# Kernel optimization log

Hardware: AMD Instinct MI355X
Metric: run time of the kernel (lower is better)

Reference implementation:

```python
import jax, jax.numpy as jnp
import numpy as np

HEADS = 8
NUM_CLASS = 4
DIM = 512


def setup_inputs() -> dict:
    key = jax.random.key(0)
    k0, k1, k2, k3 = jax.random.split(key, 4)
    B, N, C = 4, 1280, DIM  # N = (NUM_CLASS+1) * 256 tokens per group
    x = jax.random.normal(k0, (B, N, C), jnp.float32)
    # modality-presence mask: 1 = modality available, 0 = missing
    mask = jax.random.randint(k1, (B, NUM_CLASS), 0, 2).astype(jnp.int32)
    s = 1.0 / np.sqrt(C)
    W_qkv = jax.random.normal(k2, (C, 3 * C), jnp.float32) * s  # qkv (no bias)
    W_proj = jax.random.normal(k3, (C, C), jnp.float32) * s
    b_proj = jnp.zeros((C,), jnp.float32)
    return {"x": x, "mask": mask, "W_qkv": W_qkv, "W_proj": W_proj, "b_proj": b_proj}


def reference(x, mask, W_qkv, W_proj, b_proj):
    B, N, C = x.shape
    H = HEADS
    hd = C // H
    scale = hd ** -0.5
    # qkv: [B,N,3C] -> [3,B,H,N,hd]
    qkv = (x @ W_qkv).reshape(B, N, 3, H, hd).transpose(2, 0, 3, 1, 4)
    q, k, v = qkv[0], qkv[1], qkv[2]
    attn = jnp.einsum('bhqd,bhkd->bhqk', q, k) * scale  # [B,H,N,N]
    # block mask: keys belonging to missing modality groups are disallowed;
    # the last (fusion) group is always allowed -> every row has valid keys.
    np_ = N // (NUM_CLASS + 1)  # tokens per group
    group = jnp.arange(N) // np_  # [N], group id in [0, NUM_CLASS]
    allowed = jnp.concatenate(
        [mask.astype(jnp.float32), jnp.ones((B, 1), jnp.float32)], axis=1)  # [B, NUM_CLASS+1]
    col_ok = allowed[:, group]  # [B, N] per-key allowance
    attn = jnp.where(col_ok[:, None, None, :] == 0, -jnp.inf, attn)
    attn = jax.nn.softmax(attn, axis=-1)
    out = jnp.einsum('bhqk,bhkd->bhqd', attn, v)  # [B,H,N,hd]
    out = out.transpose(0, 2, 1, 3).reshape(B, N, C)
    out = out @ W_proj + b_proj
    return out, attn
```

## Files before the change

### kernel.cpp

```cpp
#include <hip/hip_runtime.h>
#include <math.h>

#define BATCH 4
#define NSEQ  1280
#define CDIM  512
#define HEADS 8
#define HD    64
#define NT    20
#define NQT   20

typedef __attribute__((ext_vector_type(8))) short bf16x8;
typedef __attribute__((ext_vector_type(4))) float f32x4;
typedef __attribute__((ext_vector_type(4))) unsigned short us4;

#define MFMA16(a,b,c) __builtin_amdgcn_mfma_f32_16x16x32_bf16(a,b,c,0,0,0)

__device__ __forceinline__ unsigned short f2bf(float f) {
    union { float f; unsigned int u; } v; v.f = f;
    unsigned int r = v.u + 0x7fffu + ((v.u >> 16) & 1u);
    return (unsigned short)(r >> 16);
}
__device__ __forceinline__ float bf2f(unsigned short h) {
    union { unsigned int u; float f; } v; v.u = ((unsigned int)h) << 16;
    return v.f;
}
__device__ __forceinline__ void gload_lds16(const void* g, void* l) {
    __builtin_amdgcn_global_load_lds(
        (const __attribute__((address_space(1))) unsigned int*)g,
        (__attribute__((address_space(3))) unsigned int*)l, 16, 0, 0);
}

__global__ __launch_bounds__(256)
void conv_kernel(const float* __restrict__ x, const float* __restrict__ Wq,
                 const float* __restrict__ Wp, unsigned short* __restrict__ xb,
                 unsigned short* __restrict__ Wqt, unsigned short* __restrict__ Wpt)
{
    __shared__ float lt[64][65];
    const int bx = blockIdx.x;
    const int tid = threadIdx.x;
    if (bx < 1280) {
        const int u = bx * 256 + tid;
        const int m = u >> 6;
        const int b6 = u & 63;
        const int chunk = b6 >> 3;
        const int blk = b6 & 7;
        const float* src = x + (size_t)m * 512 + b6 * 8;
        bf16x8 hv;
        #pragma unroll
        for (int j = 0; j < 8; ++j) hv[j] = (short)f2bf(src[j]);
        *(bf16x8*)(xb + (size_t)m * 512 + chunk * 64 + ((blk ^ (m & 7)) * 8)) = hv;
    } else {
        int wi = bx - 1280;
        const float* W; unsigned short* Wt; int N, kt, nt; bool isQ;
        if (wi < 192) { W = Wq; Wt = Wqt; N = 1536; kt = wi / 24; nt = wi % 24; isQ = true; }
        else { wi -= 192; W = Wp; Wt = Wpt; N = 512; kt = wi / 8; nt = wi % 8; isQ = false; }
        const int k0 = kt * 64, n0 = nt * 64;
        {
            const int r = tid >> 4;
            const int c = (tid & 15) * 4;
            #pragma unroll
            for (int i = 0; i < 4; ++i) {
                const float4 v = *(const float4*)(W + (size_t)(k0 + r + i * 16) * N + n0 + c);
                lt[r + i * 16][c + 0] = v.x; lt[r + i * 16][c + 1] = v.y;
                lt[r + i * 16][c + 2] = v.z; lt[r + i * 16][c + 3] = v.w;
            }
        }
        __syncthreads();
        #pragma unroll
        for (int i = 0; i < 2; ++i) {
            const int u = tid + i * 256;
            const int n = u >> 3;
            const int blk = u & 7;
            const int kin = (blk ^ (n & 7)) * 8;
            const float sc = (isQ && (n0 + n) < 512) ? 0.125f : 1.0f;
            bf16x8 o;
            #pragma unroll
            for (int j = 0; j < 8; ++j) o[j] = (short)f2bf(lt[kin + j][n] * sc);
            *(bf16x8*)(Wt + (size_t)(n0 + n) * 512 + k0 + blk * 8) = o;
        }
    }
}

template<int WM, int WN, bool BIAS, bool OUTBF16, bool SPLITV>
__global__ __launch_bounds__(256)
void gemm_bf16(const unsigned short* __restrict__ A,
               const unsigned short* __restrict__ B,
               const float* __restrict__ bias, void* __restrict__ Cv,
               unsigned short* __restrict__ Vtf,
               int M, int N, int KA, int CN)
{
    constexpr int BM = 2 * WM, BN = 2 * WN;
    constexpr int MI = WM / 16, NI = WN / 16;
    constexpr int SM0 = (BM + BN) * 64;
    constexpr int SM1 = SPLITV ? BN * (BM + 8) : 0;
    __shared__ __align__(16) unsigned short smem[SM0 > SM1 ? SM0 : SM1];
    unsigned short* As = smem;
    unsigned short* Bs = smem + BM * 64;

    const int tid = threadIdx.x;
    const int w = tid >> 6, lane = tid & 63;
    const int l15 = lane & 15, hi = lane >> 4;
    const int wr = w >> 1, wc = w & 1;

    const int nb = gridDim.x;
    const int L = (blockIdx.x & 7) * (nb >> 3) + (blockIdx.x >> 3);
    const int nx = N / BN;
    const int m0 = (L / nx) * BM, n0 = (L % nx) * BN;

    f32x4 acc[MI][NI];
    #pragma unroll
    for (int mi = 0; mi < MI; ++mi)
        #pragma unroll
        for (int ni = 0; ni < NI; ++ni) acc[mi][ni] = (f32x4){0.f, 0.f, 0.f, 0.f};

    constexpr int LA = BM * 128 / 4096;
    constexpr int LB = BN * 128 / 4096;

    for (int k0 = 0; k0 < KA; k0 += 64) {
        #pragma unroll
        for (int i = 0; i < LA; ++i) {
            const int off = tid * 16 + i * 4096;
            const int row = off >> 7, cb = off & 127;
            gload_lds16((const char*)A + ((size_t)(m0 + row) * KA + k0) * 2 + cb,
                        (char*)As + off);
        }
        #pragma unroll
        for (int i = 0; i < LB; ++i) {
            const int off = tid * 16 + i * 4096;
            const int row = off >> 7, cb = off & 127;
            gload_lds16((const char*)B + ((size_t)(n0 + row) * 512 + k0) * 2 + cb,
                        (char*)Bs + off);
        }
        __syncthreads();
        #pragma unroll
        for (int kk = 0; kk < 2; ++kk) {
            bf16x8 af[MI], bfr[NI];
            #pragma unroll
            for (int mi = 0; mi < MI; ++mi) {
                const int row = wr * WM + mi * 16 + l15;
                af[mi] = *(const bf16x8*)(As + row * 64 + ((kk * 4 + hi) ^ (row & 7)) * 8);
            }
            #pragma unroll
            for (int ni = 0; ni < NI; ++ni) {
                const int row = wc * WN + ni * 16 + l15;
                bfr[ni] = *(const bf16x8*)(Bs + row * 64 + ((kk * 4 + hi) ^ (row & 7)) * 8);
            }
            #pragma unroll
            for (int mi = 0; mi < MI; ++mi)
                #pragma unroll
                for (int ni = 0; ni < NI; ++ni)
                    acc[mi][ni] = MFMA16(af[mi], bfr[ni], acc[mi][ni]);
        }
        __syncthreads();
    }

    if (SPLITV && n0 >= 1024) {
        #pragma unroll
        for (int mi = 0; mi < MI; ++mi)
            #pragma unroll
            for (int ni = 0; ni < NI; ++ni) {
                us4 tv;
                tv[0] = f2bf(acc[mi][ni][0]); tv[1] = f2bf(acc[mi][ni][1]);
                tv[2] = f2bf(acc[mi][ni][2]); tv[3] = f2bf(acc[mi][ni][3]);
                const int col = wc * WN + ni * 16 + l15;
                *(us4*)&smem[col * (BM + 8) + wr * WM + mi * 16 + hi * 4] = tv;
            }
        __syncthreads();
        constexpr int UNITS2 = BN * (BM / 8) / 256;
        #pragma unroll
        for (int i = 0; i < UNITS2; ++i) {
            const int u = tid + i * 256;
            const int srow = u / (BM / 8), cu = u % (BM / 8);
            *(bf16x8*)(Vtf + (size_t)(n0 - 1024 + srow) * 5120 + m0 + cu * 8) =
                *(const bf16x8*)&smem[srow * (BM + 8) + cu * 8];
        }
    } else if (OUTBF16) {
        unsigned short* C = (unsigned short*)Cv;
        #pragma unroll
        for (int mi = 0; mi < MI; ++mi)
            #pragma unroll
            for (int ni = 0; ni < NI; ++ni)
                #pragma unroll
                for (int r = 0; r < 4; ++r)
                    smem[(wr * WM + mi * 16 + hi * 4 + r) * BN + wc * WN + ni * 16 + l15] =
                        f2bf(acc[mi][ni][r]);
        __syncthreads();
        constexpr int UNITS = BM * BN / 8 / 256;
        #pragma unroll
        for (int i = 0; i < UNITS; ++i) {
            const int u = tid + i * 256;
            const int row = u / (BN / 8), cb = u % (BN / 8);
            *(bf16x8*)(C + (size_t)(m0 + row) * CN + n0 + cb * 8) =
                *(const bf16x8*)(smem + row * BN + cb * 8);
        }
    } else {
        float* C = (float*)Cv;
        #pragma unroll
        for (int mi = 0; mi < MI; ++mi)
            #pragma unroll
            for (int ni = 0; ni < NI; ++ni) {
                const int col = n0 + wc * WN + ni * 16 + l15;
                const float bv = BIAS ? bias[col] : 0.f;
                #pragma unroll
                for (int r = 0; r < 4; ++r)
                    C[(size_t)(m0 + wr * WM + mi * 16 + hi * 4 + r) * CN + col] =
                        acc[mi][ni][r] + bv;
            }
    }
}

__global__ __launch_bounds__(256)
void attn_mfma(const unsigned short* __restrict__ qkb,
               const unsigned short* __restrict__ Vtf,
               const int* __restrict__ mask,
               float* __restrict__ attn, unsigned short* __restrict__ outh)
{
    __shared__ __align__(16) unsigned short kbuf[2][4096];
    __shared__ __align__(16) unsigned short vbuf[2][4096];
    __shared__ __align__(16) unsigned short psh[4096];

    const int bx = blockIdx.x;
    const int bh = bx & 31;
    const int qt = bx >> 5;
    const int b = bh >> 3, h = bh & 7;
    const int tid = threadIdx.x;
    const int w = tid >> 6;
    const int lane = tid & 63;
    const int l15 = lane & 15;
    const int hi = lane >> 4;
    const int q0 = qt * 64;

    unsigned int amask = 0xF0000u;
    #pragma unroll
    for (int g = 0; g < 4; ++g)
        if (mask[b * 4 + g] != 0) amask |= (0xFu << (g * 4));

    const unsigned short* qrow =
        qkb + (size_t)(b * NSEQ + q0 + w * 16 + l15) * 1024 + h * HD;
    const bf16x8 aq0 = *(const bf16x8*)(qrow + hi * 8);
    const bf16x8 aq1 = *(const bf16x8*)(qrow + 32 + hi * 8);

    const unsigned short* ks = qkb + (size_t)b * NSEQ * 1024 + 512 + h * HD;
    const unsigned short* vg = Vtf + (size_t)h * HD * 5120 + b * NSEQ;

    #define STAGE_K(t, buf)                                                      \
        { _Pragma("unroll")                                                      \
          for (int half_ = 0; half_ < 2; ++half_) {                              \
            const int idx_ = half_ * 256 + tid;                                  \
            const int row_ = idx_ >> 3, blk_ = idx_ & 7;                         \
            gload_lds16(ks + (size_t)((t) * 64 + row_) * 1024                    \
                           + ((blk_ ^ (row_ & 7)) * 8),                          \
                        (char*)&(buf)[0] + idx_ * 16); } }
    #define STAGE_V(t, buf)                                                      \
        { _Pragma("unroll")                                                      \
          for (int half_ = 0; half_ < 2; ++half_) {                              \
            const int idx_ = half_ * 256 + tid;                                  \
            const int row_ = idx_ >> 3, blk_ = idx_ & 7;                         \
            gload_lds16(vg + (size_t)row_ * 5120 + (t) * 64                      \
                           + ((blk_ ^ (row_ & 7)) * 8),                          \
                        (char*)&(buf)[0] + idx_ * 16); } }

    float lr[4] = {0.f, 0.f, 0.f, 0.f};

    int t0 = 0;
    while (!((amask >> t0) & 1u)) ++t0;

    STAGE_K(t0, kbuf[0]);
    __syncthreads();
    int cur = 0, t = t0;
    while (t < NT) {
        int tn = t + 1;
        while (tn < NT && !((amask >> tn) & 1u)) ++tn;
        if (tn < NT) STAGE_K(tn, kbuf[cur ^ 1]);
        f32x4 accS[4];
        #pragma unroll
        for (int cb = 0; cb < 4; ++cb) accS[cb] = (f32x4){0.f, 0.f, 0.f, 0.f};
        #pragma unroll
        for (int cb = 0; cb < 4; ++cb) {
            const int row = cb * 16 + l15;
            const char* bp = (const char*)&kbuf[cur][0] + row * 128;
            const bf16x8 b0 = *(const bf16x8*)(bp + ((hi ^ (row & 7)) * 16));
            const bf16x8 b1 = *(const bf16x8*)(bp + (((4 + hi) ^ (row & 7)) * 16));
            accS[cb] = MFMA16(aq0, b0, accS[cb]);
            accS[cb] = MFMA16(aq1, b1, accS[cb]);
        }
        #pragma unroll
        for (int cb = 0; cb < 4; ++cb)
            #pragma unroll
            for (int r = 0; r < 4; ++r)
                lr[r] += __expf(accS[cb][r]);
        __syncthreads();
        cur ^= 1; t = tn;
    }

    float rl[4];
    #pragma unroll
    for (int r = 0; r < 4; ++r) {
        float s = lr[r];
        s += __shfl_xor(s, 1);
        s += __shfl_xor(s, 2);
        s += __shfl_xor(s, 4);
        s += __shfl_xor(s, 8);
        rl[r] = 1.f / s;
    }

    {
        float* arow = attn + ((size_t)bh * NSEQ + q0 + w * 16) * NSEQ;
        const float4 z = make_float4(0.f, 0.f, 0.f, 0.f);
        for (int tz = 0; tz < NT; ++tz) {
            if ((amask >> tz) & 1u) continue;
            #pragma unroll
            for (int rr = 0; rr < 4; ++rr)
                *(float4*)(arow + (size_t)(rr * 4 + hi) * NSEQ + tz * 64 + l15 * 4) = z;
        }
    }

    STAGE_K(t0, kbuf[0]);
    STAGE_V(t0, vbuf[0]);
    __syncthreads();
    f32x4 accO[4];
    #pragma unroll
    for (int db = 0; db < 4; ++db) accO[db] = (f32x4){0.f, 0.f, 0.f, 0.f};

    cur = 0; t = t0;
    while (t < NT) {
        int tn = t + 1;
        while (tn < NT && !((amask >> tn) & 1u)) ++tn;
        if (tn < NT) {
            STAGE_K(tn, kbuf[cur ^ 1]);
            STAGE_V(tn, vbuf[cur ^ 1]);
        }
        f32x4 accS[4];
        #pragma unroll
        for (int cb = 0; cb < 4; ++cb) accS[cb] = (f32x4){0.f, 0.f, 0.f, 0.f};
        #pragma unroll
        for (int cb = 0; cb < 4; ++cb) {
            const int row = cb * 16 + l15;
            const char* bp = (const char*)&kbuf[cur][0] + row * 128;
            const bf16x8 b0 = *(const bf16x8*)(bp + ((hi ^ (row & 7)) * 16));
            const bf16x8 b1 = *(const bf16x8*)(bp + (((4 + hi) ^ (row & 7)) * 16));
            accS[cb] = MFMA16(aq0, b0, accS[cb]);
            accS[cb] = MFMA16(aq1, b1, accS[cb]);
        }

        {
            float* abase = attn + ((size_t)bh * NSEQ + q0 + w * 16) * NSEQ + t * 64;
            #pragma unroll
            for (int cb = 0; cb < 4; ++cb)
                #pragma unroll
                for (int r = 0; r < 4; ++r) {
                    const int prow = hi * 4 + r;
                    const float p = __expf(accS[cb][r]) * rl[r];
                    abase[(size_t)prow * NSEQ + cb * 16 + l15] = p;
                    const int col = cb * 16 + l15;
                    psh[(w * 16 + prow) * 64 +
                        (((col >> 3) ^ (prow & 7)) << 3) + (col & 7)] = f2bf(p);
                }
        }

        #pragma unroll
        for (int s = 0; s < 2; ++s) {
            const bf16x8 pa = *(const bf16x8*)
                &psh[(w * 16 + l15) * 64 + (((s * 4 + hi) ^ (l15 & 7)) << 3)];
            #pragma unroll
            for (int db = 0; db < 4; ++db) {
                const int row = db * 16 + l15;
                const char* bp = (const char*)&vbuf[cur][0] + row * 128;
                const bf16x8 bv = *(const bf16x8*)(bp + (((4 * s + hi) ^ (row & 7)) * 16));
                accO[db] = MFMA16(pa, bv, accO[db]);
            }
        }
        __syncthreads();
        cur ^= 1; t = tn;
    }

    #pragma unroll
    for (int db = 0; db < 4; ++db)
        #pragma unroll
        for (int r = 0; r < 4; ++r) {
            const int prow = hi * 4 + r;
            const int col = db * 16 + l15;
            psh[(w * 16 + prow) * 64 +
                (((col >> 3) ^ (prow & 7)) << 3) + (col & 7)] = f2bf(accO[db][r]);
        }
    #pragma unroll
    for (int i = 0; i < 2; ++i) {
        const int u = lane + i * 64;
        const int rowL = u >> 3;
        const int blk = u & 7;
        const bf16x8 o = *(const bf16x8*)&psh[(w * 16 + rowL) * 64 + blk * 8];
        const int n = q0 + w * 16 + rowL;
        *(bf16x8*)(outh + ((size_t)(b * NSEQ + n)) * 512 + h * 64 + blk * 8) = o;
    }
    #undef STAGE_K
    #undef STAGE_V
}

extern "C" void kernel_launch(void* const* d_in, const int* in_sizes, int n_in,
                              void* d_out, int out_size, void* d_ws, size_t ws_size,
                              hipStream_t stream)
{
    const float* x      = (const float*)d_in[0];
    const int*   mask   = (const int*)  d_in[1];
    const float* W_qkv  = (const float*)d_in[2];
    const float* W_proj = (const float*)d_in[3];
    const float* b_proj = (const float*)d_in[4];

    float* out  = (float*)d_out;
    float* attn = out + (size_t)BATCH * NSEQ * CDIM;

    char* ws = (char*)d_ws;
    unsigned short* qkb  = (unsigned short*)ws;
    unsigned short* Vtf  = qkb + (size_t)5120 * 1024;
    unsigned short* xb   = Vtf + (size_t)512 * 5120;
    unsigned short* Wqt  = xb + (size_t)5120 * 512;
    unsigned short* Wpt  = Wqt + (size_t)1536 * 512;
    unsigned short* outh = Wpt + (size_t)512 * 512;

    const int M = BATCH * NSEQ;

    conv_kernel<<<1536, 256, 0, stream>>>(x, W_qkv, W_proj, xb, Wqt, Wpt);

    gemm_bf16<64, 64, false, true, true><<<480, 256, 0, stream>>>(
        xb, Wqt, nullptr, qkb, Vtf, M, 1536, 512, 1024);

    attn_mfma<<<BATCH * HEADS * NQT, 256, 0, stream>>>(qkb, Vtf, mask, attn, outh);

    gemm_bf16<32, 64, true, false, false><<<320, 256, 0, stream>>>(
        outh, Wpt, b_proj, out, nullptr, M, 512, 512, 512);
}
```

Baseline: 86.58 us.

## Load K fragments directly from global into registers instead of LDS staging

K tiles are no longer staged into double-buffered shared memory. Each lane now loads its MFMA B-fragments for K straight from global memory into registers. This removes the K LDS buffers and the barriers in the row-sum pass, which lowers LDS use and may allow higher occupancy. In exchange the loads are no longer prefetched one tile ahead, so global latency is exposed and every wave fetches the same K rows redundantly through the cache.

```diff
diff --git a/kernel.cpp b/kernel.cpp
--- a/kernel.cpp
+++ b/kernel.cpp
@@ -215,7 +215,6 @@
                const int* __restrict__ mask,
                float* __restrict__ attn, unsigned short* __restrict__ outh)
 {
-    __shared__ __align__(16) unsigned short kbuf[2][4096];
     __shared__ __align__(16) unsigned short vbuf[2][4096];
     __shared__ __align__(16) unsigned short psh[4096];
 
@@ -243,14 +242,16 @@
     const unsigned short* ks = qkb + (size_t)b * NSEQ * 1024 + 512 + h * HD;
     const unsigned short* vg = Vtf + (size_t)h * HD * 5120 + b * NSEQ;
 
-    #define STAGE_K(t, buf)                                                      \
-        { _Pragma("unroll")                                                      \
-          for (int half_ = 0; half_ < 2; ++half_) {                              \
-            const int idx_ = half_ * 256 + tid;                                  \
-            const int row_ = idx_ >> 3, blk_ = idx_ & 7;                         \
-            gload_lds16(ks + (size_t)((t) * 64 + row_) * 1024                    \
-                           + ((blk_ ^ (row_ & 7)) * 8),                          \
-                        (char*)&(buf)[0] + idx_ * 16); } }
+    #define LOAD_KFRAGS(t)                                                       \
+        bf16x8 bk0[4], bk1[4];                                                   \
+        { const unsigned short* kt_ = ks + (size_t)(t) * 64 * 1024;              \
+          _Pragma("unroll")                                                      \
+          for (int cb_ = 0; cb_ < 4; ++cb_) {                                    \
+            const unsigned short* kr_ = kt_ + (size_t)(cb_ * 16 + l15) * 1024;   \
+            bk0[cb_] = *(const bf16x8*)(kr_ + hi * 8);                           \
+            bk1[cb_] = *(const bf16x8*)(kr_ + 32 + hi * 8);                      \
+          } }
+
     #define STAGE_V(t, buf)                                                      \
         { _Pragma("unroll")                                                      \
           for (int half_ = 0; half_ < 2; ++half_) {                              \
@@ -262,35 +263,22 @@
 
     float lr[4] = {0.f, 0.f, 0.f, 0.f};
 
-    int t0 = 0;
-    while (!((amask >> t0) & 1u)) ++t0;
-
-    STAGE_K(t0, kbuf[0]);
-    __syncthreads();
-    int cur = 0, t = t0;
-    while (t < NT) {
-        int tn = t + 1;
-        while (tn < NT && !((amask >> tn) & 1u)) ++tn;
-        if (tn < NT) STAGE_K(tn, kbuf[cur ^ 1]);
+    for (int t = 0; t < NT; ++t) {
+        if (!((amask >> t) & 1u)) continue;
+        LOAD_KFRAGS(t);
         f32x4 accS[4];
         #pragma unroll
         for (int cb = 0; cb < 4; ++cb) accS[cb] = (f32x4){0.f, 0.f, 0.f, 0.f};
         #pragma unroll
         for (int cb = 0; cb < 4; ++cb) {
-            const int row = cb * 16 + l15;
-            const char* bp = (const char*)&kbuf[cur][0] + row * 128;
-            const bf16x8 b0 = *(const bf16x8*)(bp + ((hi ^ (row & 7)) * 16));
-            const bf16x8 b1 = *(const bf16x8*)(bp + (((4 + hi) ^ (row & 7)) * 16));
-            accS[cb] = MFMA16(aq0, b0, accS[cb]);
-            accS[cb] = MFMA16(aq1, b1, accS[cb]);
+            accS[cb] = MFMA16(aq0, bk0[cb], accS[cb]);
+            accS[cb] = MFMA16(aq1, bk1[cb], accS[cb]);
         }
         #pragma unroll
         for (int cb = 0; cb < 4; ++cb)
             #pragma unroll
             for (int r = 0; r < 4; ++r)
                 lr[r] += __expf(accS[cb][r]);
-        __syncthreads();
-        cur ^= 1; t = tn;
     }
 
     float rl[4];
@@ -315,32 +303,29 @@
         }
     }
 
-    STAGE_K(t0, kbuf[0]);
+    int t0 = 0;
+    while (!((amask >> t0) & 1u)) ++t0;
+
     STAGE_V(t0, vbuf[0]);
     __syncthreads();
     f32x4 accO[4];
     #pragma unroll
     for (int db = 0; db < 4; ++db) accO[db] = (f32x4){0.f, 0.f, 0.f, 0.f};
 
-    cur = 0; t = t0;
+    int cur = 0, t = t0;
     while (t < NT) {
         int tn = t + 1;
         while (tn < NT && !((amask >> tn) & 1u)) ++tn;
-        if (tn < NT) {
-            STAGE_K(tn, kbuf[cur ^ 1]);
-            STAGE_V(tn, vbuf[cur ^ 1]);
-        }
+        if (tn < NT) STAGE_V(tn, vbuf[cur ^ 1]);
+
+        LOAD_KFRAGS(t);
         f32x4 accS[4];
         #pragma unroll
         for (int cb = 0; cb < 4; ++cb) accS[cb] = (f32x4){0.f, 0.f, 0.f, 0.f};
         #pragma unroll
         for (int cb = 0; cb < 4; ++cb) {
-            const int row = cb * 16 + l15;
-            const char* bp = (const char*)&kbuf[cur][0] + row * 128;
-            const bf16x8 b0 = *(const bf16x8*)(bp + ((hi ^ (row & 7)) * 16));
-            const bf16x8 b1 = *(const bf16x8*)(bp + (((4 + hi) ^ (row & 7)) * 16));
-            accS[cb] = MFMA16(aq0, b0, accS[cb]);
-            accS[cb] = MFMA16(aq1, b1, accS[cb]);
+            accS[cb] = MFMA16(aq0, bk0[cb], accS[cb]);
+            accS[cb] = MFMA16(aq1, bk1[cb], accS[cb]);
         }
 
         {
@@ -392,7 +377,7 @@
         const int n = q0 + w * 16 + rowL;
         *(bf16x8*)(outh + ((size_t)(b * NSEQ + n)) * 512 + h * 64 + blk * 8) = o;
     }
-    #undef STAGE_K
+    #undef LOAD_KFRAGS
     #undef STAGE_V
 }
 
```

Result: slower. 161.9 us (+87.0%).
